# Kernel tuning notes

Measured on AMD Instinct MI355X. Metric: run time of the kernel, lower is better.

## Reference

```python
import jax, jax.numpy as jnp
import numpy as np

N = 50000
E = 800000
NUM_IDS = 2048
IN_CH = 16
HID = 32
HEADS = 4
EMB = 8
GAT_IN = EMB + (IN_CH - 1)  # 23
NEG_SLOPE = 0.2


def gat_layer(x, src, dst, W, a_src, a_dst, b):
    """PyG-style GATConv (self-loops already appended to src/dst).
    x: [N, Fin]; W: [Fin, H*C]; a_src/a_dst: [H, C]; b: [H*C].
    Returns [N, H*C] (heads concatenated)."""
    H, C = a_src.shape
    h = (x @ W).reshape(-1, H, C)                      # [N,H,C]
    alpha_s = jnp.sum(h * a_src, axis=-1)              # [N,H]
    alpha_d = jnp.sum(h * a_dst, axis=-1)              # [N,H]
    e = jax.nn.leaky_relu(alpha_s[src] + alpha_d[dst], NEG_SLOPE)  # [E',H]
    # segment softmax over destination neighborhoods
    m = jax.ops.segment_max(e, dst, num_segments=N)    # [N,H]
    ex = jnp.exp(e - m[dst])
    denom = jax.ops.segment_sum(ex, dst, num_segments=N)
    alpha = ex / (denom[dst] + 1e-16)                  # [E',H]
    msg = h[src] * alpha[:, :, None]                   # [E',H,C]
    out = jax.ops.segment_sum(msg, dst, num_segments=N)  # [N,H,C]
    return out.reshape(-1, H * C) + b


def setup_inputs() -> dict:
    key = jax.random.key(0)
    ks = jax.random.split(key, 20)
    node_ids = jax.random.randint(ks[0], (N,), 0, NUM_IDS, dtype=jnp.int32)
    node_feats = jax.random.normal(ks[1], (N, IN_CH - 1), dtype=jnp.float32)
    src = jax.random.randint(ks[2], (E,), 0, N, dtype=jnp.int32)
    off = jax.random.randint(ks[3], (E,), 1, N, dtype=jnp.int32)
    dst = (src + off) % N  # guarantee no pre-existing self-loops
    edge_index = jnp.stack([src, dst]).astype(jnp.int32)
    batch = jnp.zeros((N,), dtype=jnp.int32)

    def w(k, shape):
        return jax.random.normal(k, shape, dtype=jnp.float32) * 0.1

    emb = w(ks[4], (NUM_IDS, EMB))
    # enc1: GAT_IN -> HID, heads=HEADS
    W1, a1s, a1d, b1 = w(ks[5], (GAT_IN, HEADS * HID)), w(ks[6], (HEADS, HID)), w(ks[7], (HEADS, HID)), jnp.zeros((HEADS * HID,), jnp.float32)
    # enc2: HID*HEADS -> HID, heads=1
    W2, a2s, a2d, b2 = w(ks[8], (HEADS * HID, HID)), w(ks[9], (1, HID)), w(ks[10], (1, HID)), jnp.zeros((HID,), jnp.float32)
    # dec1: HID -> HID, heads=HEADS
    W3, a3s, a3d, b3 = w(ks[11], (HID, HEADS * HID)), w(ks[12], (HEADS, HID)), w(ks[13], (HEADS, HID)), jnp.zeros((HEADS * HID,), jnp.float32)
    # dec2: HID*HEADS -> IN_CH, heads=1
    W4, a4s, a4d, b4 = w(ks[14], (HEADS * HID, IN_CH)), w(ks[15], (1, IN_CH)), w(ks[16], (1, IN_CH)), jnp.zeros((IN_CH,), jnp.float32)
    return {"node_ids": node_ids, "node_feats": node_feats, "edge_index": edge_index,
            "batch": batch, "emb": emb,
            "W1": W1, "a1s": a1s, "a1d": a1d, "b1": b1,
            "W2": W2, "a2s": a2s, "a2d": a2d, "b2": b2,
            "W3": W3, "a3s": a3s, "a3d": a3d, "b3": b3,
            "W4": W4, "a4s": a4s, "a4d": a4d, "b4": b4}


def reference(node_ids, node_feats, edge_index, batch, emb,
              W1, a1s, a1d, b1, W2, a2s, a2d, b2,
              W3, a3s, a3d, b3, W4, a4s, a4d, b4):
    # PyG GATConv adds self-loops by default
    loop = jnp.arange(N, dtype=edge_index.dtype)
    src = jnp.concatenate([edge_index[0], loop])
    dst = jnp.concatenate([edge_index[1], loop])
    x = jnp.concatenate([emb[node_ids], node_feats], axis=1)  # [N, GAT_IN]
    x = jax.nn.relu(gat_layer(x, src, dst, W1, a1s, a1d, b1))
    x = jax.nn.relu(gat_layer(x, src, dst, W2, a2s, a2d, b2))
    x = jax.nn.relu(gat_layer(x, src, dst, W3, a3s, a3d, b3))
    x = jax.nn.sigmoid(gat_layer(x, src, dst, W4, a4s, a4d, b4))
    return x
```

## Files before the change

kernel.cpp:

```cpp
#include <hip/hip_runtime.h>
#include <hip/hip_bf16.h>

typedef __hip_bfloat16 bf16;
typedef float f32x2 __attribute__((ext_vector_type(2)));

#define NEG_SLOPE 0.2f
#define DCAP 128

__device__ __forceinline__ float lrelu(float x) { return fmaxf(x, NEG_SLOPE * x); }
__device__ __forceinline__ f32x2 bfp(unsigned pv) {
    f32x2 r;
    r.x = __uint_as_float(pv << 16);
    r.y = __uint_as_float(pv & 0xffff0000u);
    return r;
}
__device__ __forceinline__ void fma8p(f32x2* acc, float w, uint4 pv) {
    f32x2 wv = {w, w};
    acc[0] += wv * bfp(pv.x);
    acc[1] += wv * bfp(pv.y);
    acc[2] += wv * bfp(pv.z);
    acc[3] += wv * bfp(pv.w);
}
__device__ __forceinline__ ushort bfbits(float x) {
    bf16 b = __float2bfloat16(x);
    return *reinterpret_cast<ushort*>(&b);
}

static inline int cdiv(int a, int b) { return (a + b - 1) / b; }
__host__ __device__ static inline int imin(int a, int b) { return a < b ? a : b; }

__global__ void fill_sentinel(float* __restrict__ y, int n) {
    int t = blockIdx.x * 256 + threadIdx.x;
    if (t < n) y[t] = 2.0f;
}

__global__ __launch_bounds__(256) void init_and_t1(
    int* __restrict__ cursor, int IB,
    const int* __restrict__ ids, const float* __restrict__ feats,
    const float* __restrict__ emb, const float* __restrict__ W1,
    const float* __restrict__ a1s, const float* __restrict__ a1d,
    bf16* __restrict__ h_out, float* __restrict__ as_out, float* __restrict__ ad_out, int N) {
    if ((int)blockIdx.x < IB) {
        int i = blockIdx.x * 256 + threadIdx.x;
        if (i < N) cursor[i] = i * DCAP;
        return;
    }
    constexpr int FIN = 23, FINP = 27, HC = 128;
    __shared__ float xs[2 * FINP];
    const int node0 = (blockIdx.x - IB) * 2;
    const int tid = threadIdx.x;
    if (tid < 2 * FIN) {
        int ln = tid / FIN, f = tid - ln * FIN;
        int i = node0 + ln;
        float v = 0.f;
        if (i < N) v = (f < 8) ? emb[ids[i] * 8 + f] : feats[i * 15 + (f - 8)];
        xs[ln * FINP + f] = v;
    }
    __syncthreads();
    const int ln = tid >> 7, j = tid & 127;
    const int i = node0 + ln;
    if (i >= N) return;
    float acc = 0.f;
#pragma unroll
    for (int f = 0; f < FIN; ++f) acc += xs[ln * FINP + f] * W1[f * HC + j];
    h_out[(size_t)i * HC + j] = __float2bfloat16(acc);
    float s = acc * a1s[j];
    float d = acc * a1d[j];
#pragma unroll
    for (int off = 16; off > 0; off >>= 1) {
        s += __shfl_down(s, off, 32);
        d += __shfl_down(d, off, 32);
    }
    if ((j & 31) == 0) {
        as_out[i * 4 + j / 32] = s;
        ad_out[i * 4 + j / 32] = d;
    }
}

template <typename EIDX>
__global__ void fill_direct(const int* __restrict__ src, const int* __restrict__ dst,
                            int* __restrict__ cursor, EIDX* __restrict__ elsrc, int E) {
    int t = blockIdx.x * 256 + threadIdx.x;
    if (t >= E) return;
    int d = dst[t];
    int slot = atomicAdd(&cursor[d], 1);
    if (slot < d * DCAP + DCAP) elsrc[slot] = (EIDX)src[t];
}

template <int H, int C, int HN, int CN, bool FINAL, typename EIDX>
__global__ __launch_bounds__(256) void gat_tf(
    const int* __restrict__ cursor, const EIDX* __restrict__ elsrc,
    const bf16* __restrict__ hIn, const float* __restrict__ asIn,
    const float* __restrict__ adIn, const float* __restrict__ bias,
    const float* __restrict__ Wn, const float* __restrict__ anS,
    const float* __restrict__ anD, bf16* __restrict__ hOut,
    float* __restrict__ asOut, float* __restrict__ adOut,
    float* __restrict__ yout, int N) {
    constexpr int HC = H * C;
    constexpr int HCN = HN * CN;
    constexpr int LPR = HC / 8;
    constexpr int EPI = 64 / LPR;
    constexpr int HCP = HC + 4;
    __shared__ int src_s[256];
    __shared__ float w_s[256 * H];
    __shared__ float xs[FINAL ? 1 : 4 * HCP];
    const int wvi = threadIdx.x >> 6;
    const int lane = threadIdx.x & 63;
    const int step = gridDim.x * 4;
    const int grp = lane / LPR;
    const int lin = lane - grp * LPR;
    const int ch0 = 8 * lin;
    const int h0 = ch0 / C;

    for (int d = blockIdx.x * 4 + wvi; d < N; d += step) {
        const int row = d * DCAP;
        const int s_pre = (int)elsrc[row + lane];
        const int end = imin(cursor[d], row + DCAP);
        float ad_d[H], c[H], den_p[H];
        if constexpr (H == 4) {
            float4 adv = *(const float4*)(adIn + d * 4);
            float4 asv = *(const float4*)(asIn + d * 4);
            ad_d[0] = adv.x; ad_d[1] = adv.y; ad_d[2] = adv.z; ad_d[3] = adv.w;
            c[0] = lrelu(asv.x + adv.x);
            c[1] = lrelu(asv.y + adv.y);
            c[2] = lrelu(asv.z + adv.z);
            c[3] = lrelu(asv.w + adv.w);
            den_p[0] = den_p[1] = den_p[2] = den_p[3] = 0.f;
        } else {
            ad_d[0] = adIn[d];
            c[0] = lrelu(asIn[d] + ad_d[0]);
            den_p[0] = 0.f;
        }
        f32x2 acc[4];
#pragma unroll
        for (int q = 0; q < 4; ++q) acc[q] = (f32x2){0.f, 0.f};
        if (grp == 0) {
            uint4 pv = *(const uint4*)(hIn + (size_t)d * HC + ch0);
            acc[0] = bfp(pv.x);
            acc[1] = bfp(pv.y);
            acc[2] = bfp(pv.z);
            acc[3] = bfp(pv.w);
        }
        for (int base = row; base < end; base += 64) {
            int e = base + lane;
            int s = (base == row) ? s_pre : ((e < end) ? (int)elsrc[e] : -1);
            if (e >= end) s = -1;
            if constexpr (H == 4) {
                float4 w4 = {0.f, 0.f, 0.f, 0.f};
                if (s >= 0) {
                    float4 av = *(const float4*)(asIn + s * 4);
                    w4.x = __expf(lrelu(av.x + ad_d[0]) - c[0]);
                    w4.y = __expf(lrelu(av.y + ad_d[1]) - c[1]);
                    w4.z = __expf(lrelu(av.z + ad_d[2]) - c[2]);
                    w4.w = __expf(lrelu(av.w + ad_d[3]) - c[3]);
                    den_p[0] += w4.x;
                    den_p[1] += w4.y;
                    den_p[2] += w4.z;
                    den_p[3] += w4.w;
                }
                *(float4*)&w_s[(wvi * 64 + lane) * 4] = w4;
            } else {
                float w0 = 0.f;
                if (s >= 0) {
                    w0 = __expf(lrelu(asIn[s] + ad_d[0]) - c[0]);
                    den_p[0] += w0;
                }
                w_s[wvi * 64 + lane] = w0;
            }
            src_s[wvi * 64 + lane] = (s >= 0) ? s : 0;
            int nv = imin(64, end - base);
#pragma unroll 4
            for (int k0 = 0; k0 < nv; k0 += EPI) {
                int k = k0 + grp;
                if (k < nv) {
                    int sk = src_s[wvi * 64 + k];
                    float w = w_s[(wvi * 64 + k) * H + h0];
                    uint4 pv = *(const uint4*)(hIn + (size_t)sk * HC + ch0);
                    fma8p(acc, w, pv);
                }
            }
        }
#pragma unroll
        for (int h = 0; h < H; ++h) {
            float v = den_p[h];
#pragma unroll
            for (int o = 32; o > 0; o >>= 1) v += __shfl_xor(v, o, 64);
            den_p[h] = v + 1.0f;
        }
#pragma unroll
        for (int o = LPR; o < 64; o <<= 1) {
#pragma unroll
            for (int q = 0; q < 4; ++q) {
                acc[q].x += __shfl_xor(acc[q].x, o, 64);
                acc[q].y += __shfl_xor(acc[q].y, o, 64);
            }
        }
        if (grp == 0) {
            float inv = 1.f / (den_p[h0] + 1e-16f);
            float v[8];
#pragma unroll
            for (int q = 0; q < 4; ++q) {
                v[2 * q] = acc[q].x * inv + bias[ch0 + 2 * q];
                v[2 * q + 1] = acc[q].y * inv + bias[ch0 + 2 * q + 1];
            }
            if constexpr (FINAL) {
                float4 o0, o1;
                o0.x = 1.f / (1.f + __expf(-v[0]));
                o0.y = 1.f / (1.f + __expf(-v[1]));
                o0.z = 1.f / (1.f + __expf(-v[2]));
                o0.w = 1.f / (1.f + __expf(-v[3]));
                o1.x = 1.f / (1.f + __expf(-v[4]));
                o1.y = 1.f / (1.f + __expf(-v[5]));
                o1.z = 1.f / (1.f + __expf(-v[6]));
                o1.w = 1.f / (1.f + __expf(-v[7]));
                *(float4*)(yout + (size_t)d * HC + ch0) = o0;
                *(float4*)(yout + (size_t)d * HC + ch0 + 4) = o1;
            } else {
#pragma unroll
                for (int r = 0; r < 8; ++r)
                    xs[wvi * HCP + ch0 + r] = v[r] > 0.f ? v[r] : 0.f;
            }
        }

        if constexpr (!FINAL) {
            __builtin_amdgcn_wave_barrier();
            const float* xrow = xs + wvi * HCP;
            constexpr int PJ = HCN / 2;
            constexpr int SEG = 64 / PJ;
            constexpr int FSEG = HC / SEG;
            constexpr int PPH = CN / 2;
            const int jp = lane % PJ;
            const int seg = lane / PJ;
            const int f0 = seg * FSEG;
            f32x2 ab = {0.f, 0.f};
#pragma unroll
            for (int f = 0; f < FSEG; f += 4) {
                float4 xv = *(const float4*)&xrow[f0 + f];
                f32x2 w0 = *(const f32x2*)&Wn[(f0 + f + 0) * HCN + 2 * jp];
                f32x2 w1 = *(const f32x2*)&Wn[(f0 + f + 1) * HCN + 2 * jp];
                f32x2 w2 = *(const f32x2*)&Wn[(f0 + f + 2) * HCN + 2 * jp];
                f32x2 w3 = *(const f32x2*)&Wn[(f0 + f + 3) * HCN + 2 * jp];
                ab += (f32x2){xv.x, xv.x} * w0;
                ab += (f32x2){xv.y, xv.y} * w1;
                ab += (f32x2){xv.z, xv.z} * w2;
                ab += (f32x2){xv.w, xv.w} * w3;
            }
#pragma unroll
            for (int o = PJ; o < 64; o <<= 1) {
                ab.x += __shfl_xor(ab.x, o, 64);
                ab.y += __shfl_xor(ab.y, o, 64);
            }
            if (seg == 0) {
                ushort2 st;
                st.x = bfbits(ab.x);
                st.y = bfbits(ab.y);
                *(ushort2*)(hOut + (size_t)d * HCN + 2 * jp) = st;
            }
            float2 aS = *(const float2*)&anS[2 * jp];
            float2 aD = *(const float2*)&anD[2 * jp];
            float sv = ab.x * aS.x + ab.y * aS.y;
            float dv = ab.x * aD.x + ab.y * aD.y;
#pragma unroll
            for (int o = PPH / 2; o > 0; o >>= 1) {
                sv += __shfl_down(sv, o, PPH);
                dv += __shfl_down(dv, o, PPH);
            }
            if (seg == 0 && (jp % PPH) == 0) {
                asOut[d * HN + jp / PPH] = sv;
                adOut[d * HN + jp / PPH] = dv;
            }
        }
    }
}

template <typename EIDX>
static void run_layers(const int* cursor, const EIDX* elsrc, bf16* hA, bf16* hB,
                       float* asA, float* adA, float* asB, float* adB, float* y,
                       void* const* d_in, int N, hipStream_t stream) {
    const float* b1 = (const float*)d_in[8];
    const float* W2 = (const float*)d_in[9];
    const float* a2s = (const float*)d_in[10];
    const float* a2d = (const float*)d_in[11];
    const float* b2 = (const float*)d_in[12];
    const float* W3 = (const float*)d_in[13];
    const float* a3s = (const float*)d_in[14];
    const float* a3d = (const float*)d_in[15];
    const float* b3 = (const float*)d_in[16];
    const float* W4 = (const float*)d_in[17];
    const float* a4s = (const float*)d_in[18];
    const float* a4d = (const float*)d_in[19];
    const float* b4 = (const float*)d_in[20];
    const int g = imin(2048, cdiv(N, 4));
    gat_tf<4, 32, 1, 32, false, EIDX><<<g, 256, 0, stream>>>(
        cursor, elsrc, hA, asA, adA, b1, W2, a2s, a2d, hB, asB, adB, y, N);
    gat_tf<1, 32, 4, 32, false, EIDX><<<g, 256, 0, stream>>>(
        cursor, elsrc, hB, asB, adB, b2, W3, a3s, a3d, hA, asA, adA, y, N);
    gat_tf<4, 32, 1, 16, false, EIDX><<<g, 256, 0, stream>>>(
        cursor, elsrc, hA, asA, adA, b3, W4, a4s, a4d, hB, asB, adB, y, N);
    gat_tf<1, 16, 1, 1, true, EIDX><<<g, 256, 0, stream>>>(
        cursor, elsrc, hB, asB, adB, b4, W4, a4s, a4d, hA, asA, adA, y, N);
}

extern "C" void kernel_launch(void* const* d_in, const int* in_sizes, int n_in,
                              void* d_out, int out_size, void* d_ws, size_t ws_size,
                              hipStream_t stream) {
    const int N = in_sizes[0];
    const int E = in_sizes[2] / 2;
    const int* node_ids = (const int*)d_in[0];
    const float* feats = (const float*)d_in[1];
    const int* srcI = (const int*)d_in[2];
    const int* dstI = srcI + E;
    const float* emb = (const float*)d_in[4];
    const float* W1 = (const float*)d_in[5];
    const float* a1s = (const float*)d_in[6];
    const float* a1d = (const float*)d_in[7];
    float* y = (float*)d_out;

    float* asA = (float*)d_ws;
    float* adA = asA + (size_t)N * 4;
    float* asB = adA + (size_t)N * 4;
    float* adB = asB + (size_t)N * 4;
    bf16* hA = (bf16*)(adB + (size_t)N * 4);
    bf16* hB = hA + (size_t)N * 128;
    int* cursor = (int*)(hB + (size_t)N * 128);
    int* elsrc = cursor + N;

    const bool u16 = (N <= 65536);
    size_t elsz = (size_t)N * DCAP * (u16 ? 2 : 4);
    size_t need = (size_t)N * 4 * 4 * 4 + (size_t)N * 128 * 2 * 2 + (size_t)N * 4 + elsz;
    if (ws_size < need) {
        fill_sentinel<<<cdiv(out_size, 256), 256, 0, stream>>>(y, out_size);
        return;
    }

    const int IB = cdiv(N, 256);
    init_and_t1<<<IB + cdiv(N, 2), 256, 0, stream>>>(cursor, IB, node_ids, feats, emb,
                                                     W1, a1s, a1d, hA, asA, adA, N);
    if (u16) {
        ushort* el16 = (ushort*)elsrc;
        fill_direct<ushort><<<cdiv(E, 256), 256, 0, stream>>>(srcI, dstI, cursor, el16, E);
        run_layers<ushort>(cursor, el16, hA, hB, asA, adA, asB, adB, y, d_in, N, stream);
    } else {
        fill_direct<int><<<cdiv(E, 256), 256, 0, stream>>>(srcI, dstI, cursor, elsrc, E);
        run_layers<int>(cursor, elsrc, hA, hB, asA, adA, asB, adB, y, d_in, N, stream);
    }
}
```

Measured before the change: 396.0 us.

## Stage GAT weights in LDS and launch one block per four nodes

Copies the next-layer weight matrix, attention vectors and bias into shared memory at the start of each block, and stages W1 in shared memory in the first layer kernel. It drops the grid-stride loop so each block processes exactly four destination nodes, with the grid sized to cover all nodes. The aim is to replace repeated global weight reads with LDS reads. In exchange, every small block reloads the full weight matrix and adds a block barrier and more LDS, which may reduce occupancy.

After: 380.0 us. 1.04x faster.

```diff
diff --git a/kernel.cpp b/kernel.cpp
--- a/kernel.cpp
+++ b/kernel.cpp
@@ -47,8 +47,11 @@
     }
     constexpr int FIN = 23, FINP = 27, HC = 128;
     __shared__ float xs[2 * FINP];
+    __shared__ __align__(16) float w1_s[FIN * HC];
     const int node0 = (blockIdx.x - IB) * 2;
     const int tid = threadIdx.x;
+    for (int i = tid; i < FIN * HC / 4; i += 256)
+        ((float4*)w1_s)[i] = ((const float4*)W1)[i];
     if (tid < 2 * FIN) {
         int ln = tid / FIN, f = tid - ln * FIN;
         int i = node0 + ln;
@@ -62,7 +65,7 @@
     if (i >= N) return;
     float acc = 0.f;
 #pragma unroll
-    for (int f = 0; f < FIN; ++f) acc += xs[ln * FINP + f] * W1[f * HC + j];
+    for (int f = 0; f < FIN; ++f) acc += xs[ln * FINP + f] * w1_s[f * HC + j];
     h_out[(size_t)i * HC + j] = __float2bfloat16(acc);
     float s = acc * a1s[j];
     float d = acc * a1d[j];
@@ -104,15 +107,31 @@
     __shared__ int src_s[256];
     __shared__ float w_s[256 * H];
     __shared__ float xs[FINAL ? 1 : 4 * HCP];
-    const int wvi = threadIdx.x >> 6;
-    const int lane = threadIdx.x & 63;
-    const int step = gridDim.x * 4;
+    __shared__ __align__(16) float wn_s[FINAL ? 4 : HC * HCN];
+    __shared__ __align__(16) float an_s[FINAL ? 4 : 2 * HCN];
+    __shared__ float bias_s[HC];
+    const int tid = threadIdx.x;
+    if constexpr (!FINAL) {
+        for (int i = tid; i < HC * HCN / 4; i += 256)
+            ((float4*)wn_s)[i] = ((const float4*)Wn)[i];
+        if (tid < HCN) {
+            an_s[tid] = anS[tid];
+            an_s[HCN + tid] = anD[tid];
+        }
+    }
+    if (tid < HC) bias_s[tid] = bias[tid];
+    __syncthreads();
+
+    const int wvi = tid >> 6;
+    const int lane = tid & 63;
+    const int d = blockIdx.x * 4 + wvi;
+    if (d >= N) return;
     const int grp = lane / LPR;
     const int lin = lane - grp * LPR;
     const int ch0 = 8 * lin;
     const int h0 = ch0 / C;
 
-    for (int d = blockIdx.x * 4 + wvi; d < N; d += step) {
+    {
         const int row = d * DCAP;
         const int s_pre = (int)elsrc[row + lane];
         const int end = imin(cursor[d], row + DCAP);
@@ -200,8 +219,8 @@
             float v[8];
 #pragma unroll
             for (int q = 0; q < 4; ++q) {
-                v[2 * q] = acc[q].x * inv + bias[ch0 + 2 * q];
-                v[2 * q + 1] = acc[q].y * inv + bias[ch0 + 2 * q + 1];
+                v[2 * q] = acc[q].x * inv + bias_s[ch0 + 2 * q];
+                v[2 * q + 1] = acc[q].y * inv + bias_s[ch0 + 2 * q + 1];
             }
             if constexpr (FINAL) {
                 float4 o0, o1;
@@ -221,54 +240,52 @@
                     xs[wvi * HCP + ch0 + r] = v[r] > 0.f ? v[r] : 0.f;
             }
         }
-
-        if constexpr (!FINAL) {
-            __builtin_amdgcn_wave_barrier();
-            const float* xrow = xs + wvi * HCP;
-            constexpr int PJ = HCN / 2;
-            constexpr int SEG = 64 / PJ;
-            constexpr int FSEG = HC / SEG;
-            constexpr int PPH = CN / 2;
-            const int jp = lane % PJ;
-            const int seg = lane / PJ;
-            const int f0 = seg * FSEG;
-            f32x2 ab = {0.f, 0.f};
-#pragma unroll
-            for (int f = 0; f < FSEG; f += 4) {
-                float4 xv = *(const float4*)&xrow[f0 + f];
-                f32x2 w0 = *(const f32x2*)&Wn[(f0 + f + 0) * HCN + 2 * jp];
-                f32x2 w1 = *(const f32x2*)&Wn[(f0 + f + 1) * HCN + 2 * jp];
-                f32x2 w2 = *(const f32x2*)&Wn[(f0 + f + 2) * HCN + 2 * jp];
-                f32x2 w3 = *(const f32x2*)&Wn[(f0 + f + 3) * HCN + 2 * jp];
-                ab += (f32x2){xv.x, xv.x} * w0;
-                ab += (f32x2){xv.y, xv.y} * w1;
-                ab += (f32x2){xv.z, xv.z} * w2;
-                ab += (f32x2){xv.w, xv.w} * w3;
-            }
-#pragma unroll
-            for (int o = PJ; o < 64; o <<= 1) {
-                ab.x += __shfl_xor(ab.x, o, 64);
-                ab.y += __shfl_xor(ab.y, o, 64);
-            }
-            if (seg == 0) {
-                ushort2 st;
-                st.x = bfbits(ab.x);
-                st.y = bfbits(ab.y);
-                *(ushort2*)(hOut + (size_t)d * HCN + 2 * jp) = st;
-            }
-            float2 aS = *(const float2*)&anS[2 * jp];
-            float2 aD = *(const float2*)&anD[2 * jp];
-            float sv = ab.x * aS.x + ab.y * aS.y;
-            float dv = ab.x * aD.x + ab.y * aD.y;
-#pragma unroll
-            for (int o = PPH / 2; o > 0; o >>= 1) {
-                sv += __shfl_down(sv, o, PPH);
-                dv += __shfl_down(dv, o, PPH);
-            }
-            if (seg == 0 && (jp % PPH) == 0) {
-                asOut[d * HN + jp / PPH] = sv;
-                adOut[d * HN + jp / PPH] = dv;
-            }
+    }
+
+    if constexpr (!FINAL) {
+        __builtin_amdgcn_wave_barrier();
+        const float* xrow = xs + wvi * HCP;
+        constexpr int PJ = HCN / 2;
+        constexpr int SEG = 64 / PJ;
+        constexpr int FSEG = HC / SEG;
+        constexpr int PPH = CN / 2;
+        const int jp = lane % PJ;
+        const int seg = lane / PJ;
+        const int f0 = seg * FSEG;
+        float a0 = 0.f, a1 = 0.f;
+#pragma unroll
+        for (int f = 0; f < FSEG; f += 4) {
+            float4 xv = *(const float4*)&xrow[f0 + f];
+            float2 w0 = *(const float2*)&wn_s[(f0 + f + 0) * HCN + 2 * jp];
+            float2 w1 = *(const float2*)&wn_s[(f0 + f + 1) * HCN + 2 * jp];
+            float2 w2 = *(const float2*)&wn_s[(f0 + f + 2) * HCN + 2 * jp];
+            float2 w3 = *(const float2*)&wn_s[(f0 + f + 3) * HCN + 2 * jp];
+            a0 += xv.x * w0.x + xv.y * w1.x + xv.z * w2.x + xv.w * w3.x;
+            a1 += xv.x * w0.y + xv.y * w1.y + xv.z * w2.y + xv.w * w3.y;
+        }
+#pragma unroll
+        for (int o = PJ; o < 64; o <<= 1) {
+            a0 += __shfl_xor(a0, o, 64);
+            a1 += __shfl_xor(a1, o, 64);
+        }
+        if (seg == 0) {
+            ushort2 st;
+            st.x = bfbits(a0);
+            st.y = bfbits(a1);
+            *(ushort2*)(hOut + (size_t)d * HCN + 2 * jp) = st;
+        }
+        float2 aS = *(const float2*)&an_s[2 * jp];
+        float2 aD = *(const float2*)&an_s[HCN + 2 * jp];
+        float sv = a0 * aS.x + a1 * aS.y;
+        float dv = a0 * aD.x + a1 * aD.y;
+#pragma unroll
+        for (int o = PPH / 2; o > 0; o >>= 1) {
+            sv += __shfl_down(sv, o, PPH);
+            dv += __shfl_down(dv, o, PPH);
+        }
+        if (seg == 0 && (jp % PPH) == 0) {
+            asOut[d * HN + jp / PPH] = sv;
+            adOut[d * HN + jp / PPH] = dv;
         }
     }
 }
@@ -290,7 +307,7 @@
     const float* a4s = (const float*)d_in[18];
     const float* a4d = (const float*)d_in[19];
     const float* b4 = (const float*)d_in[20];
-    const int g = imin(2048, cdiv(N, 4));
+    const int g = cdiv(N, 4);
     gat_tf<4, 32, 1, 32, false, EIDX><<<g, 256, 0, stream>>>(
         cursor, elsrc, hA, asA, adA, b1, W2, a2s, a2d, hB, asB, adB, y, N);
     gat_tf<1, 32, 4, 32, false, EIDX><<<g, 256, 0, stream>>>(
```
